# Kernel optimization log

Measured on AMD Instinct MI355X. Metric: run time of the kernel, lower is better.

Reference implementation:

```python
import jax, jax.numpy as jnp
import numpy as np

D_MODEL = 1024
HEADS = 16
DEPTH = D_MODEL // HEADS
B, S = 4, 4096
EPS_K = 1e-6  # kernel feature epsilon
EPS_LN = 1e-6


def setup_inputs() -> dict:
    key = jax.random.key(0)
    ks = jax.random.split(key, 8)
    lecun = 1.0 / np.sqrt(D_MODEL)  # LecunNormal stddev
    glorot = np.sqrt(2.0 / (D_MODEL + D_MODEL))  # keras Dense default
    return {
        "q": jax.random.normal(ks[0], (B, S, D_MODEL), jnp.float32),
        "k": jax.random.normal(ks[1], (B, S, D_MODEL), jnp.float32),
        "v": jax.random.normal(ks[2], (B, S, D_MODEL), jnp.float32),
        "mask": jnp.ones((B, S), jnp.float32),
        "wq": jax.random.normal(ks[3], (D_MODEL, D_MODEL), jnp.float32) * lecun,
        "wk": jax.random.normal(ks[4], (D_MODEL, D_MODEL), jnp.float32) * lecun,
        "wv": jax.random.normal(ks[5], (D_MODEL, D_MODEL), jnp.float32) * lecun,
        "ln_gamma": jnp.ones((D_MODEL,), jnp.float32),
        "ln_beta": jnp.zeros((D_MODEL,), jnp.float32),
        "dense_w": jax.random.normal(ks[6], (D_MODEL, D_MODEL), jnp.float32) * glorot,
        "dense_b": jnp.zeros((D_MODEL,), jnp.float32),
    }


def _layernorm(x, g, b):
    m = jnp.mean(x, axis=-1, keepdims=True)
    var = jnp.var(x, axis=-1, keepdims=True)
    return (x - m) * jax.lax.rsqrt(var + EPS_LN) * g + b


def _split_heads(x):
    bsz, sl, _ = x.shape
    return x.reshape(bsz, sl, HEADS, DEPTH).transpose(0, 2, 1, 3)  # [B,H,S,depth]


def reference(q, k, v, mask, wq, wk, wv, ln_gamma, ln_beta, dense_w, dense_b):
    bsz = q.shape[0]
    em = mask[:, None, :, None]  # [B,1,S,1] broadcast over heads/depth
    qh = _split_heads(_layernorm(q @ wq, ln_gamma, ln_beta))
    kh = _split_heads(_layernorm(k @ wk, ln_gamma, ln_beta))
    vh = _split_heads(_layernorm(v @ wv, ln_gamma, ln_beta))
    q_prime = jax.nn.relu(qh) + EPS_K
    k_prime = (jax.nn.relu(kh) + EPS_K) * em
    vh = vh * em
    kv = jnp.einsum('bhnd,bhne->bhde', k_prime, vh)  # [B,H,depth,depth]
    z = 1.0 / (jnp.einsum('bhnd,bhd->bhn', q_prime, k_prime.sum(axis=-2)) + EPS_K)
    att = jnp.einsum('bhnd,bhde,bhn->bhne', q_prime, kv, z)  # [B,H,S,depth]
    # Faithful to original: reshape WITHOUT transposing heads back.
    att = att.reshape(bsz, -1, D_MODEL)  # [B,S,d_model]
    out = att @ dense_w + dense_b
    return _layernorm(out, ln_gamma, ln_beta)
```

## Files before the change

### kernel.cpp

```cpp
#include <hip/hip_runtime.h>
#include <hip/hip_bf16.h>
#include <stdint.h>

#define D_MODEL 1024
#define S_LEN   4096
#define BATCH   4
#define HEADS   16
#define DEPTH   64
#define ROWS    (BATCH*S_LEN)
#define EPS_K_F 1e-6f
#define EPS_LN_F 1e-6f

typedef __attribute__((ext_vector_type(8))) short short8;
typedef __attribute__((ext_vector_type(4))) float f32x4;

__device__ __forceinline__ unsigned short f2bf(float f) {
  union { float f; unsigned u; } x; x.f = f;
  unsigned r = x.u + 0x7FFF + ((x.u >> 16) & 1);
  return (unsigned short)(r >> 16);
}
__device__ __forceinline__ float bf2f(unsigned short b) {
  union { unsigned u; float f; } x; x.u = ((unsigned)b) << 16;
  return x.f;
}
__device__ __forceinline__ void gload16(const void* g, void* l) {
  __builtin_amdgcn_global_load_lds(
      (const __attribute__((address_space(1))) void*)g,
      (__attribute__((address_space(3))) void*)l, 16, 0, 0);
}

__global__ __launch_bounds__(256) void cvt3_k(
    const float* __restrict__ q, const float* __restrict__ k,
    const float* __restrict__ v,
    unsigned short* __restrict__ xq, unsigned short* __restrict__ xk,
    unsigned short* __restrict__ xv, int nb_per) {
  int tb = blockIdx.x / nb_per;
  int i = (blockIdx.x % nb_per) * 256 + threadIdx.x;
  const float* src = (tb == 0) ? q : (tb == 1) ? k : v;
  unsigned short* dst = (tb == 0) ? xq : (tb == 1) ? xk : xv;
  float4 val = ((const float4*)src)[i];
  ushort4 o;
  o.x = f2bf(val.x); o.y = f2bf(val.y); o.z = f2bf(val.z); o.w = f2bf(val.w);
  ((ushort4*)dst)[i] = o;
}

__global__ __launch_bounds__(256) void wtrans_k(
    const float* __restrict__ W, unsigned short* __restrict__ Wt) {
  __shared__ float tile[32][33];
  int n0 = blockIdx.x * 32, k0 = blockIdx.y * 32;
  int tx = threadIdx.x & 31, ty = threadIdx.x >> 5;
  #pragma unroll
  for (int i = 0; i < 32; i += 8)
    tile[ty + i][tx] = W[(size_t)(k0 + ty + i) * D_MODEL + n0 + tx];
  __syncthreads();
  #pragma unroll
  for (int i = 0; i < 32; i += 8)
    Wt[(size_t)(n0 + ty + i) * D_MODEL + k0 + tx] = f2bf(tile[tx][ty + i]);
}


#define GEMM_EPILOGUE(HASBIAS)                                               \
  if (HASBIAS) {                                                             \
    float bv[4];                                                             \
    _Pragma("unroll")                                                        \
    for (int n = 0; n < 4; ++n)                                              \
      bv[n] = bias[(int)n0 + wcn * 64 + n * 16 + l15];                       \
    _Pragma("unroll")                                                        \
    for (int m = 0; m < 8; ++m)                                              \
      _Pragma("unroll")                                                      \
      for (int n = 0; n < 4; ++n)                                            \
        _Pragma("unroll")                                                    \
        for (int j = 0; j < 4; ++j)                                          \
          acc[m][n][j] += bv[n];                                             \
  }                                                                          \
  int seg = (int)(n0 >> 6) + wcn;                                            \
  _Pragma("unroll")                                                          \
  for (int m = 0; m < 8; ++m) {                                              \
    float s[4], s2[4];                                                       \
    _Pragma("unroll")                                                        \
    for (int j = 0; j < 4; ++j) {                                            \
      float a = 0.f, b = 0.f;                                                \
      _Pragma("unroll")                                                      \
      for (int n = 0; n < 4; ++n) { float x = acc[m][n][j]; a += x; b += x*x; } \
      s[j] = a; s2[j] = b;                                                   \
    }                                                                        \
    _Pragma("unroll")                                                        \
    for (int off = 1; off < 16; off <<= 1) {                                 \
      _Pragma("unroll")                                                      \
      for (int j = 0; j < 4; ++j) {                                          \
        s[j]  += __shfl_xor(s[j],  off);                                     \
        s2[j] += __shfl_xor(s2[j], off);                                     \
      }                                                                      \
    }                                                                        \
    if (l15 == 0) {                                                          \
      _Pragma("unroll")                                                      \
      for (int j = 0; j < 4; ++j) {                                          \
        int rg = (int)m0 + wr * 128 + m * 16 + lhi * 4 + j;                  \
        psum[rg * 16 + seg] = s[j];                                          \
        psq [rg * 16 + seg] = s2[j];                                         \
      }                                                                      \
    }                                                                        \
  }                                                                          \
  _Pragma("unroll")                                                          \
  for (int m = 0; m < 8; ++m)                                                \
    _Pragma("unroll")                                                        \
    for (int j = 0; j < 4; ++j) {                                            \
      size_t row = m0 + wr * 128 + m * 16 + lhi * 4 + j;                     \
      _Pragma("unroll")                                                      \
      for (int n = 0; n < 4; ++n) {                                          \
        int col = (int)n0 + wcn * 64 + n * 16 + l15;                         \
        Cb[row * N + col] = f2bf(acc[m][n][j]);                              \
      }                                                                      \
    }

#define STAGE_HALF(kof_, slot_, h_) do {                                     \
    _Pragma("unroll")                                                        \
    for (int j = 0; j < 2; ++j) {                                            \
      int idx = j * 512 + t; int r_ = idx >> 2; int cs_ = idx & 3;           \
      int c_ = cs_ ^ (r_ & 3);                                               \
      gload16(A + (m0 + r_) * (size_t)K + (kof_) + (h_) * 32 + c_ * 8,       \
              &Al[slot_][(h_) * 8192 + idx * 8]);                            \
    }                                                                        \
    _Pragma("unroll")                                                        \
    for (int j = 0; j < 2; ++j) {                                            \
      int idx = j * 512 + t; int r_ = idx >> 2; int cs_ = idx & 3;           \
      int c_ = cs_ ^ (r_ & 3);                                               \
      gload16(Bt + (n0 + r_) * (size_t)K + (kof_) + (h_) * 32 + c_ * 8,      \
              &Bl[slot_][(h_) * 8192 + idx * 8]);                            \
    }                                                                        \
  } while (0)

#define PH_READ_B(kk_)                                                       \
    _Pragma("unroll")                                                        \
    for (int n = 0; n < 4; ++n) {                                            \
      int rb_ = wcn * 64 + n * 16 + l15;                                     \
      bfr[n] = *(const short8*)&Bl[slot][(kk_) * 8192 + rb_ * 32 + cswz];    \
    }
#define PH_READ_A(kk_, mh_)                                                  \
    _Pragma("unroll")                                                        \
    for (int m = 0; m < 4; ++m) {                                            \
      int ra_ = wr * 128 + ((mh_) * 4 + m) * 16 + l15;                       \
      af[m] = *(const short8*)&Al[slot][(kk_) * 8192 + ra_ * 32 + cswz];     \
    }
#define PH_MFMA(mh_)                                                         \
    __builtin_amdgcn_s_setprio(1);                                           \
    _Pragma("unroll")                                                        \
    for (int m = 0; m < 4; ++m)                                              \
      _Pragma("unroll")                                                      \
      for (int n = 0; n < 4; ++n)                                            \
        acc[(mh_) * 4 + m][n] = __builtin_amdgcn_mfma_f32_16x16x32_bf16(     \
            af[m], bfr[n], acc[(mh_) * 4 + m][n], 0, 0, 0);                  \
    __builtin_amdgcn_s_setprio(0);
#define LGKM0                                                                \
    asm volatile("s_waitcnt lgkmcnt(0)" ::: "memory");                       \
    __builtin_amdgcn_sched_barrier(0);

__global__ __launch_bounds__(512, 2) void gemm_bt_k(
    const unsigned short* __restrict__ A,
    const unsigned short* __restrict__ Bt,
    unsigned short* __restrict__ Cb,
    float* __restrict__ psum, float* __restrict__ psq,
    const float* __restrict__ bias,
    int M, int N, int K) {
  __shared__ unsigned short Al[2][16384];
  __shared__ unsigned short Bl[2][16384];
  int t = threadIdx.x;
  int lane = t & 63, wid = t >> 6;
  int wr = wid >> 2, wcn = wid & 3;
  int l15 = lane & 15, lhi = lane >> 4;
  const int cswz = (lhi ^ (l15 & 3)) << 3;
  int p = blockIdx.x;
  int cb = (p >> 3) & 3;
  int rb = (p & 7) | ((p >> 5) << 3);
  size_t m0 = (size_t)rb * 256, n0 = (size_t)cb * 256;
  f32x4 acc[8][4] = {};

  const int KT = K >> 6;

  STAGE_HALF(0, 0, 0);  STAGE_HALF(0, 0, 1);
  STAGE_HALF(64, 1, 0); STAGE_HALF(64, 1, 1);
  asm volatile("s_waitcnt vmcnt(8)" ::: "memory");
  __builtin_amdgcn_s_barrier();
  __builtin_amdgcn_sched_barrier(0);

  for (int kt = 0; kt < KT; ++kt) {
    const int slot = kt & 1;
    short8 af[4], bfr[4];
    PH_READ_B(0)
    PH_READ_A(0, 0)
    LGKM0
    PH_MFMA(0)
    PH_READ_A(0, 1)
    LGKM0
    __builtin_amdgcn_s_barrier();
    __builtin_amdgcn_sched_barrier(0);
    if (kt + 2 < KT) STAGE_HALF((kt + 2) << 6, slot, 0);
    __builtin_amdgcn_sched_barrier(0);
    PH_MFMA(1)
    PH_READ_B(1)
    PH_READ_A(1, 0)
    LGKM0
    PH_MFMA(0)
    PH_READ_A(1, 1)
    LGKM0
    __builtin_amdgcn_s_barrier();
    __builtin_amdgcn_sched_barrier(0);
    if (kt + 2 < KT) STAGE_HALF((kt + 2) << 6, slot, 1);
    __builtin_amdgcn_sched_barrier(0);
    PH_MFMA(1)
    if (kt + 1 < KT) {
      if (kt + 2 < KT)
        asm volatile("s_waitcnt vmcnt(8)" ::: "memory");
      else
        asm volatile("s_waitcnt vmcnt(0)" ::: "memory");
      __builtin_amdgcn_s_barrier();
      __builtin_amdgcn_sched_barrier(0);
    }
  }

  GEMM_EPILOGUE(bias != nullptr)
}

__global__ __launch_bounds__(256) void ln_act_k(
    const unsigned short* __restrict__ Cb,
    const float* __restrict__ psum, const float* __restrict__ psq,
    const float* __restrict__ gamma, const float* __restrict__ beta,
    const float* __restrict__ mask,
    unsigned short* __restrict__ out, int mode) {
  int row = blockIdx.x;
  int t = threadIdx.x;
  float s = 0.f, s2 = 0.f;
  #pragma unroll
  for (int i = 0; i < 16; ++i) { s += psum[row * 16 + i]; s2 += psq[row * 16 + i]; }
  float mean = s * (1.f / D_MODEL);
  float var = s2 * (1.f / D_MODEL) - mean * mean;
  float rstd = rsqrtf(var + EPS_LN_F);
  float mk = (mode > 0) ? mask[row] : 1.f;
  ushort4 cv = ((const ushort4*)(Cb + (size_t)row * D_MODEL))[t];
  float4 gv = ((const float4*)gamma)[t];
  float4 bv = ((const float4*)beta)[t];
  float av[4] = {bf2f(cv.x), bf2f(cv.y), bf2f(cv.z), bf2f(cv.w)};
  float g4[4] = {gv.x, gv.y, gv.z, gv.w};
  float b4[4] = {bv.x, bv.y, bv.z, bv.w};
  unsigned short ov[4];
  #pragma unroll
  for (int j = 0; j < 4; ++j) {
    float ln = (av[j] - mean) * rstd * g4[j] + b4[j];
    if (mode == 0)      ln = fmaxf(ln, 0.f) + EPS_K_F;
    else if (mode == 1) ln = (fmaxf(ln, 0.f) + EPS_K_F) * mk;
    else                ln = ln * mk;
    ov[j] = f2bf(ln);
  }
  ushort4 o; o.x = ov[0]; o.y = ov[1]; o.z = ov[2]; o.w = ov[3];
  ((ushort4*)(out + (size_t)row * D_MODEL))[t] = o;
}

__global__ __launch_bounds__(256) void ln_final_k(
    const unsigned short* __restrict__ Cb,
    const float* __restrict__ psum, const float* __restrict__ psq,
    const float* __restrict__ gamma, const float* __restrict__ beta,
    float* __restrict__ out) {
  int row = blockIdx.x;
  int t = threadIdx.x;
  float s = 0.f, s2 = 0.f;
  #pragma unroll
  for (int i = 0; i < 16; ++i) { s += psum[row * 16 + i]; s2 += psq[row * 16 + i]; }
  float mean = s * (1.f / D_MODEL);
  float var = s2 * (1.f / D_MODEL) - mean * mean;
  float rstd = rsqrtf(var + EPS_LN_F);
  ushort4 cv = ((const ushort4*)(Cb + (size_t)row * D_MODEL))[t];
  float4 gv = ((const float4*)gamma)[t];
  float4 bv = ((const float4*)beta)[t];
  float4 w;
  w.x = (bf2f(cv.x) - mean) * rstd * gv.x + bv.x;
  w.y = (bf2f(cv.y) - mean) * rstd * gv.y + bv.y;
  w.z = (bf2f(cv.z) - mean) * rstd * gv.z + bv.z;
  w.w = (bf2f(cv.w) - mean) * rstd * gv.w + bv.w;
  ((float4*)(out + (size_t)row * D_MODEL))[t] = w;
}

__global__ __launch_bounds__(256) void kv_mfma_k(
    const unsigned short* __restrict__ Kp, const unsigned short* __restrict__ Vp,
    float* __restrict__ part, float* __restrict__ kspart) {
  __shared__ unsigned short Kl[4096];
  __shared__ unsigned short Vl[4096];
  int bh = blockIdx.y, chunk = blockIdx.x;
  int b_ = bh >> 4, h = bh & 15;
  int t = threadIdx.x, lane = t & 63, w = t >> 6;
  int l15 = lane & 15, g = lane >> 4;

  int sn = t >> 2, sd16 = t & 3;
  int sc = sd16 ^ ((sn >> 3) & 3);
  size_t goff = (size_t)sn * D_MODEL + h * DEPTH + sd16 * 16;
  int ldst = sn * 64 + sc * 16;

  short8 ones;
  #pragma unroll
  for (int i = 0; i < 8; ++i) ones[i] = (short)0x3F80;

  f32x4 acc[4] = {};
  f32x4 ks = {};

  int baseA = ((w ^ g) << 4) + l15;
  int baseB0 = ((0 ^ g) << 4) + l15;
  int baseB1 = ((1 ^ g) << 4) + l15;
  int baseB2 = ((2 ^ g) << 4) + l15;
  int baseB3 = ((3 ^ g) << 4) + l15;

  size_t rowbase = ((size_t)b_ * S_LEN + (size_t)chunk * 512) * D_MODEL;
  for (int tile = 0; tile < 8; ++tile) {
    const unsigned short* kg = Kp + rowbase + (size_t)tile * 64 * D_MODEL + goff;
    const unsigned short* vg = Vp + rowbase + (size_t)tile * 64 * D_MODEL + goff;
    uint4 ra = *(const uint4*)kg;
    uint4 rb = *(const uint4*)(kg + 8);
    uint4 rc = *(const uint4*)vg;
    uint4 rd = *(const uint4*)(vg + 8);
    __syncthreads();
    *(uint4*)&Kl[ldst]     = ra;
    *(uint4*)&Kl[ldst + 8] = rb;
    *(uint4*)&Vl[ldst]     = rc;
    *(uint4*)&Vl[ldst + 8] = rd;
    __syncthreads();
    #pragma unroll
    for (int kk = 0; kk < 2; ++kk) {
      int nb = (kk * 32 + g * 8) * 64;
      short8 af, bf0, bf1, bf2, bf3;
      #pragma unroll
      for (int i = 0; i < 8; ++i) {
        int rowoff = nb + i * 64;
        af[i]  = (short)Kl[rowoff + baseA];
        bf0[i] = (short)Vl[rowoff + baseB0];
        bf1[i] = (short)Vl[rowoff + baseB1];
        bf2[i] = (short)Vl[rowoff + baseB2];
        bf3[i] = (short)Vl[rowoff + baseB3];
      }
      acc[0] = __builtin_amdgcn_mfma_f32_16x16x32_bf16(af, bf0, acc[0], 0, 0, 0);
      acc[1] = __builtin_amdgcn_mfma_f32_16x16x32_bf16(af, bf1, acc[1], 0, 0, 0);
      acc[2] = __builtin_amdgcn_mfma_f32_16x16x32_bf16(af, bf2, acc[2], 0, 0, 0);
      acc[3] = __builtin_amdgcn_mfma_f32_16x16x32_bf16(af, bf3, acc[3], 0, 0, 0);
      ks     = __builtin_amdgcn_mfma_f32_16x16x32_bf16(af, ones, ks, 0, 0, 0);
    }
  }
  float* pp = part + ((size_t)bh * 8 + chunk) * 4096;
  #pragma unroll
  for (int nf = 0; nf < 4; ++nf)
    #pragma unroll
    for (int r = 0; r < 4; ++r)
      pp[(16 * w + 4 * g + r) * 64 + 16 * nf + l15] = acc[nf][r];
  if (l15 == 0) {
    #pragma unroll
    for (int r = 0; r < 4; ++r)
      kspart[((size_t)bh * 8 + chunk) * 64 + 16 * w + 4 * g + r] = ks[r];
  }
}

__global__ __launch_bounds__(256) void kv_reduce_k(
    const float* __restrict__ part, const float* __restrict__ kspart,
    unsigned short* __restrict__ KVT, float* __restrict__ ksum) {
  int bh = blockIdx.x, t = threadIdx.x;
  for (int idx = t; idx < 4096; idx += 256) {
    int d = idx >> 6, e = idx & 63;
    float s = 0.f;
    #pragma unroll
    for (int c = 0; c < 8; ++c)
      s += part[((size_t)bh * 8 + c) * 4096 + d * 64 + e];
    KVT[(size_t)bh * 4096 + e * 64 + d] = f2bf(s);
  }
  if (t < 64) {
    float s = 0.f;
    #pragma unroll
    for (int c = 0; c < 8; ++c) s += kspart[((size_t)bh * 8 + c) * 64 + t];
    ksum[bh * 64 + t] = s;
  }
}

__global__ __launch_bounds__(256) void att_k(
    const unsigned short* __restrict__ Qp, const unsigned short* __restrict__ KVT,
    const float* __restrict__ ksum, unsigned short* __restrict__ att) {
  __shared__ unsigned short Ql[128 * 64];
  __shared__ unsigned short Kl[64 * 64];
  __shared__ float ksl[64];
  __shared__ float zl[128];
  int bh = blockIdx.y;
  int b = bh >> 4, h = bh & 15;
  int r0 = blockIdx.x * 128;
  int t = threadIdx.x, lane = t & 63, wid = t >> 6;
  int l15 = lane & 15, lhi = lane >> 4;
  #pragma unroll
  for (int i = 0; i < 4; ++i) {
    int cid = i * 256 + t;
    int r = cid >> 3, c8 = cid & 7;
    gload16(Qp + ((size_t)(b * S_LEN + r0 + r)) * D_MODEL + h * DEPTH + c8 * 8,
            &Ql[cid * 8]);
  }
  #pragma unroll
  for (int i = 0; i < 2; ++i) {
    int cid = i * 256 + t;
    gload16(KVT + (size_t)bh * 4096 + cid * 8, &Kl[cid * 8]);
  }
  if (t < 64) ksl[t] = ksum[bh * 64 + t];
  asm volatile("s_waitcnt vmcnt(0)" ::: "memory");
  __syncthreads();
  {
    int r = t >> 1, half = t & 1;
    float s = 0.f;
    #pragma unroll
    for (int j = 0; j < 32; ++j)
      s += bf2f(Ql[r * 64 + half * 32 + j]) * ksl[half * 32 + j];
    s += __shfl_xor(s, 1);
    if (half == 0) zl[r] = 1.f / (s + EPS_K_F);
  }
  __syncthreads();
  f32x4 acc[2][4] = {};
  #pragma unroll
  for (int kk = 0; kk < 2; ++kk) {
    short8 af[2], bfr[4];
    #pragma unroll
    for (int m = 0; m < 2; ++m)
      af[m] = *(const short8*)&Ql[(wid * 32 + m * 16 + l15) * 64 + kk * 32 + lhi * 8];
    #pragma unroll
    for (int n = 0; n < 4; ++n)
      bfr[n] = *(const short8*)&Kl[(n * 16 + l15) * 64 + kk * 32 + lhi * 8];
    #pragma unroll
    for (int m = 0; m < 2; ++m)
      #pragma unroll
      for (int n = 0; n < 4; ++n)
        acc[m][n] = __builtin_amdgcn_mfma_f32_16x16x32_bf16(af[m], bfr[n], acc[m][n], 0, 0, 0);
  }
  #pragma unroll
  for (int m = 0; m < 2; ++m)
    #pragma unroll
    for (int j = 0; j < 4; ++j) {
      int rl = wid * 32 + m * 16 + lhi * 4 + j;
      int n = r0 + rl;
      float z = zl[rl];
      #pragma unroll
      for (int nf = 0; nf < 4; ++nf) {
        int ee = nf * 16 + l15;
        size_t orow = (size_t)b * S_LEN + h * 256 + (n >> 4);
        int ocol = (n & 15) * 64 + ee;
        att[orow * D_MODEL + ocol] = f2bf(acc[m][nf][j] * z);
      }
    }
}

extern "C" void kernel_launch(void* const* d_in, const int* in_sizes, int n_in,
                              void* d_out, int out_size, void* d_ws, size_t ws_size,
                              hipStream_t stream) {
  (void)in_sizes; (void)n_in; (void)out_size; (void)ws_size;
  const float* q     = (const float*)d_in[0];
  const float* k     = (const float*)d_in[1];
  const float* v     = (const float*)d_in[2];
  const float* mask  = (const float*)d_in[3];
  const float* wq    = (const float*)d_in[4];
  const float* wk    = (const float*)d_in[5];
  const float* wv    = (const float*)d_in[6];
  const float* gamma = (const float*)d_in[7];
  const float* beta  = (const float*)d_in[8];
  const float* dw    = (const float*)d_in[9];
  const float* db    = (const float*)d_in[10];
  float* out = (float*)d_out;

  char* ws = (char*)d_ws;
  unsigned short* Xq  = (unsigned short*)(ws);
  unsigned short* Xk  = (unsigned short*)(ws + 33554432);
  unsigned short* Xv  = (unsigned short*)(ws + 67108864);
  unsigned short* Qp  = Xq;
  unsigned short* Kp  = Xk;
  unsigned short* Vp  = Xv;
  unsigned short* Cd  = Xq;
  unsigned short* WqT = (unsigned short*)(ws + 100663296);
  unsigned short* WkT = WqT + 1048576;
  unsigned short* WvT = WkT + 1048576;
  unsigned short* WdT = WvT + 1048576;
  float* part   = (float*)(ws + 109051904);
  float* kspart = (float*)(ws + 117440512);
  unsigned short* KVT = (unsigned short*)(ws + 117964800);
  float* ksum = (float*)(ws + 118489088);
  float* psum = (float*)(ws + 119537664);
  float* psq  = (float*)(ws + 120586240);
  unsigned short* Cqkv = (unsigned short*)d_out;

  dim3 b256(256);
  dim3 b512(512);
  int n4 = ROWS * D_MODEL / 4;
  int nb_per = n4 / 256;
  dim3 wtg(32, 32);
  dim3 gemmg(256);
  dim3 lng(ROWS);

  wtrans_k<<<wtg, b256, 0, stream>>>(wq, WqT);
  wtrans_k<<<wtg, b256, 0, stream>>>(wk, WkT);
  wtrans_k<<<wtg, b256, 0, stream>>>(wv, WvT);
  wtrans_k<<<wtg, b256, 0, stream>>>(dw, WdT);

  cvt3_k<<<dim3(3 * nb_per), b256, 0, stream>>>(q, k, v, Xq, Xk, Xv, nb_per);

  gemm_bt_k<<<gemmg, b512, 0, stream>>>(Xq, WqT, Cqkv, psum, psq, nullptr,
                                        ROWS, D_MODEL, D_MODEL);
  ln_act_k<<<lng, b256, 0, stream>>>(Cqkv, psum, psq, gamma, beta, nullptr, Qp, 0);

  gemm_bt_k<<<gemmg, b512, 0, stream>>>(Xk, WkT, Cqkv, psum, psq, nullptr,
                                        ROWS, D_MODEL, D_MODEL);
  ln_act_k<<<lng, b256, 0, stream>>>(Cqkv, psum, psq, gamma, beta, mask, Kp, 1);

  gemm_bt_k<<<gemmg, b512, 0, stream>>>(Xv, WvT, Cqkv, psum, psq, nullptr,
                                        ROWS, D_MODEL, D_MODEL);
  ln_act_k<<<lng, b256, 0, stream>>>(Cqkv, psum, psq, gamma, beta, mask, Vp, 2);

  kv_mfma_k<<<dim3(8, 64), b256, 0, stream>>>(Kp, Vp, part, kspart);
  kv_reduce_k<<<dim3(64), b256, 0, stream>>>(part, kspart, KVT, ksum);
  att_k<<<dim3(32, 64), b256, 0, stream>>>(Qp, KVT, ksum, Cqkv);

  gemm_bt_k<<<gemmg, b512, 0, stream>>>(Cqkv, WdT, Cd, psum, psq, db,
                                        ROWS, D_MODEL, D_MODEL);
  ln_final_k<<<lng, b256, 0, stream>>>(Cd, psum, psq, gamma, beta, out);
}
```

Before: 360.5 us.

## Overlap fp32-to-bf16 conversion of next input inside projection GEMM main loop

The k and v conversions to bf16 move out of the standalone conversion kernel and into the preceding projection GEMM. Each block loads and packs a slice of the next tensor between k-tiles, so the bandwidth-bound conversion can hide behind MFMA work. The main loop is peeled to drop the per-iteration bounds checks, and vmcnt waits are adjusted for the extra side loads. The min-blocks hint of 2 in launch_bounds is also removed, which may change register allocation and occupancy. The added global traffic and registers could slow the GEMM.

```diff
diff --git a/kernel.cpp b/kernel.cpp
--- a/kernel.cpp
+++ b/kernel.cpp
@@ -29,19 +29,15 @@
       (__attribute__((address_space(3))) void*)l, 16, 0, 0);
 }
 
-__global__ __launch_bounds__(256) void cvt3_k(
-    const float* __restrict__ q, const float* __restrict__ k,
-    const float* __restrict__ v,
-    unsigned short* __restrict__ xq, unsigned short* __restrict__ xk,
-    unsigned short* __restrict__ xv, int nb_per) {
-  int tb = blockIdx.x / nb_per;
-  int i = (blockIdx.x % nb_per) * 256 + threadIdx.x;
-  const float* src = (tb == 0) ? q : (tb == 1) ? k : v;
-  unsigned short* dst = (tb == 0) ? xq : (tb == 1) ? xk : xv;
-  float4 val = ((const float4*)src)[i];
-  ushort4 o;
-  o.x = f2bf(val.x); o.y = f2bf(val.y); o.z = f2bf(val.z); o.w = f2bf(val.w);
-  ((ushort4*)dst)[i] = o;
+__global__ __launch_bounds__(256) void cvt_f32_bf16_k(
+    const float* __restrict__ in, unsigned short* __restrict__ out, int n4) {
+  int i = blockIdx.x * 256 + threadIdx.x;
+  if (i < n4) {
+    float4 v = ((const float4*)in)[i];
+    ushort4 o;
+    o.x = f2bf(v.x); o.y = f2bf(v.y); o.z = f2bf(v.z); o.w = f2bf(v.w);
+    ((ushort4*)out)[i] = o;
+  }
 }
 
 __global__ __launch_bounds__(256) void wtrans_k(
@@ -155,12 +151,37 @@
     asm volatile("s_waitcnt lgkmcnt(0)" ::: "memory");                       \
     __builtin_amdgcn_sched_barrier(0);
 
-__global__ __launch_bounds__(512, 2) void gemm_bt_k(
+#define SIDE_PACK_STORE(chunk_) do {                                         \
+    uint4 pk_;                                                               \
+    pk_.x = (unsigned)f2bf(sreg0.x) | ((unsigned)f2bf(sreg0.y) << 16);       \
+    pk_.y = (unsigned)f2bf(sreg0.z) | ((unsigned)f2bf(sreg0.w) << 16);       \
+    pk_.z = (unsigned)f2bf(sreg1.x) | ((unsigned)f2bf(sreg1.y) << 16);       \
+    pk_.w = (unsigned)f2bf(sreg1.z) | ((unsigned)f2bf(sreg1.w) << 16);       \
+    *(uint4*)(side_dst + sbase + (size_t)(chunk_) * 4096) = pk_;             \
+  } while (0)
+#define SIDE_LOAD(chunk_) do {                                               \
+    const float* sp_ = side_src + sbase + (size_t)(chunk_) * 4096;           \
+    sreg0 = *(const float4*)sp_; sreg1 = *(const float4*)(sp_ + 4);          \
+  } while (0)
+
+#define TAIL_TILE(slot_) do {                                                \
+    const int slot = (slot_);                                                \
+    short8 af[4], bfr[4];                                                    \
+    PH_READ_B(0) PH_READ_A(0, 0) LGKM0 PH_MFMA(0)                            \
+    PH_READ_A(0, 1) LGKM0 PH_MFMA(1)                                         \
+    PH_READ_B(1) PH_READ_A(1, 0) LGKM0 PH_MFMA(0)                            \
+    PH_READ_A(1, 1) LGKM0 PH_MFMA(1)                                         \
+  } while (0)
+
+template <bool SIDECAR>
+__global__ __launch_bounds__(512) void gemm_bt_k(
     const unsigned short* __restrict__ A,
     const unsigned short* __restrict__ Bt,
     unsigned short* __restrict__ Cb,
     float* __restrict__ psum, float* __restrict__ psq,
     const float* __restrict__ bias,
+    const float* __restrict__ side_src,
+    unsigned short* __restrict__ side_dst,
     int M, int N, int K) {
   __shared__ unsigned short Al[2][16384];
   __shared__ unsigned short Bl[2][16384];
@@ -177,13 +198,17 @@
 
   const int KT = K >> 6;
 
+  float4 sreg0 = {}, sreg1 = {};
+  size_t sbase = (size_t)p * 65536 + (size_t)t * 8;
+
+  if (SIDECAR) SIDE_LOAD(0);
   STAGE_HALF(0, 0, 0);  STAGE_HALF(0, 0, 1);
   STAGE_HALF(64, 1, 0); STAGE_HALF(64, 1, 1);
   asm volatile("s_waitcnt vmcnt(8)" ::: "memory");
   __builtin_amdgcn_s_barrier();
   __builtin_amdgcn_sched_barrier(0);
 
-  for (int kt = 0; kt < KT; ++kt) {
+  for (int kt = 0; kt < KT - 2; ++kt) {
     const int slot = kt & 1;
     short8 af[4], bfr[4];
     PH_READ_B(0)
@@ -194,7 +219,7 @@
     LGKM0
     __builtin_amdgcn_s_barrier();
     __builtin_amdgcn_sched_barrier(0);
-    if (kt + 2 < KT) STAGE_HALF((kt + 2) << 6, slot, 0);
+    STAGE_HALF((kt + 2) << 6, slot, 0);
     __builtin_amdgcn_sched_barrier(0);
     PH_MFMA(1)
     PH_READ_B(1)
@@ -205,18 +230,35 @@
     LGKM0
     __builtin_amdgcn_s_barrier();
     __builtin_amdgcn_sched_barrier(0);
-    if (kt + 2 < KT) STAGE_HALF((kt + 2) << 6, slot, 1);
+    STAGE_HALF((kt + 2) << 6, slot, 1);
     __builtin_amdgcn_sched_barrier(0);
     PH_MFMA(1)
-    if (kt + 1 < KT) {
-      if (kt + 2 < KT)
-        asm volatile("s_waitcnt vmcnt(8)" ::: "memory");
-      else
-        asm volatile("s_waitcnt vmcnt(0)" ::: "memory");
-      __builtin_amdgcn_s_barrier();
+    if (SIDECAR) {
+      SIDE_PACK_STORE(kt);
+      SIDE_LOAD(kt + 1);
       __builtin_amdgcn_sched_barrier(0);
+      asm volatile("s_waitcnt vmcnt(11)" ::: "memory");
+    } else {
+      asm volatile("s_waitcnt vmcnt(8)" ::: "memory");
     }
-  }
+    __builtin_amdgcn_s_barrier();
+    __builtin_amdgcn_sched_barrier(0);
+  }
+
+  TAIL_TILE((KT - 2) & 1);
+  if (SIDECAR) {
+    SIDE_PACK_STORE(KT - 2);
+    SIDE_LOAD(KT - 1);
+    __builtin_amdgcn_sched_barrier(0);
+    asm volatile("s_waitcnt vmcnt(3)" ::: "memory");
+  } else {
+    asm volatile("s_waitcnt vmcnt(0)" ::: "memory");
+  }
+  __builtin_amdgcn_s_barrier();
+  __builtin_amdgcn_sched_barrier(0);
+
+  TAIL_TILE((KT - 1) & 1);
+  if (SIDECAR) SIDE_PACK_STORE(KT - 1);
 
   GEMM_EPILOGUE(bias != nullptr)
 }
@@ -484,7 +526,7 @@
   dim3 b256(256);
   dim3 b512(512);
   int n4 = ROWS * D_MODEL / 4;
-  int nb_per = n4 / 256;
+  dim3 cvtg(n4 / 256);
   dim3 wtg(32, 32);
   dim3 gemmg(256);
   dim3 lng(ROWS);
@@ -494,25 +536,25 @@
   wtrans_k<<<wtg, b256, 0, stream>>>(wv, WvT);
   wtrans_k<<<wtg, b256, 0, stream>>>(dw, WdT);
 
-  cvt3_k<<<dim3(3 * nb_per), b256, 0, stream>>>(q, k, v, Xq, Xk, Xv, nb_per);
-
-  gemm_bt_k<<<gemmg, b512, 0, stream>>>(Xq, WqT, Cqkv, psum, psq, nullptr,
-                                        ROWS, D_MODEL, D_MODEL);
+  cvt_f32_bf16_k<<<cvtg, b256, 0, stream>>>(q, Xq, n4);
+
+  gemm_bt_k<true><<<gemmg, b512, 0, stream>>>(Xq, WqT, Cqkv, psum, psq, nullptr,
+                                              k, Xk, ROWS, D_MODEL, D_MODEL);
   ln_act_k<<<lng, b256, 0, stream>>>(Cqkv, psum, psq, gamma, beta, nullptr, Qp, 0);
 
-  gemm_bt_k<<<gemmg, b512, 0, stream>>>(Xk, WkT, Cqkv, psum, psq, nullptr,
-                                        ROWS, D_MODEL, D_MODEL);
+  gemm_bt_k<true><<<gemmg, b512, 0, stream>>>(Xk, WkT, Cqkv, psum, psq, nullptr,
+                                              v, Xv, ROWS, D_MODEL, D_MODEL);
   ln_act_k<<<lng, b256, 0, stream>>>(Cqkv, psum, psq, gamma, beta, mask, Kp, 1);
 
-  gemm_bt_k<<<gemmg, b512, 0, stream>>>(Xv, WvT, Cqkv, psum, psq, nullptr,
-                                        ROWS, D_MODEL, D_MODEL);
+  gemm_bt_k<false><<<gemmg, b512, 0, stream>>>(Xv, WvT, Cqkv, psum, psq, nullptr,
+                                               nullptr, nullptr, ROWS, D_MODEL, D_MODEL);
   ln_act_k<<<lng, b256, 0, stream>>>(Cqkv, psum, psq, gamma, beta, mask, Vp, 2);
 
   kv_mfma_k<<<dim3(8, 64), b256, 0, stream>>>(Kp, Vp, part, kspart);
   kv_reduce_k<<<dim3(64), b256, 0, stream>>>(part, kspart, KVT, ksum);
   att_k<<<dim3(32, 64), b256, 0, stream>>>(Qp, KVT, ksum, Cqkv);
 
-  gemm_bt_k<<<gemmg, b512, 0, stream>>>(Cqkv, WdT, Cd, psum, psq, db,
-                                        ROWS, D_MODEL, D_MODEL);
+  gemm_bt_k<false><<<gemmg, b512, 0, stream>>>(Cqkv, WdT, Cd, psum, psq, db,
+                                               nullptr, nullptr, ROWS, D_MODEL, D_MODEL);
   ln_final_k<<<lng, b256, 0, stream>>>(Cd, psum, psq, gamma, beta, out);
 }
```

New measurement: 353.3 us. -2.0%, faster.
